# Performance work log

Measured on AMD Instinct MI355X. Metric: run time of the kernel, lower is better.

The kernel has to match this reference:

```python
import jax, jax.numpy as jnp
import numpy as np

KERNEL = 3
STRIDE = 1
PADDING = 1
DILATION = 1
GRID_SIZE = 3
SPLINE_ORDER = 2
IN_CH = 3
OUT_CH = 32
IN_FEAT = IN_CH * KERNEL * KERNEL  # 27
N_BASIS = GRID_SIZE + SPLINE_ORDER  # 5


def _make_grid():
    # efficient-kan grid: uniform knots over [-1, 1] extended by spline_order on each side
    h = 2.0 / GRID_SIZE
    g = np.arange(-SPLINE_ORDER, GRID_SIZE + SPLINE_ORDER + 1, dtype=np.float32) * h - 1.0
    return jnp.asarray(np.broadcast_to(g, (IN_FEAT, g.shape[0])))  # (27, 8)


def b_splines(x, grid):
    # x: (N, F); grid: (F, G). Cox-de Boor recursion.
    x = x[:, :, None]                      # (N, F, 1)
    g = grid[None, :, :]                   # (1, F, G)
    bases = ((x >= g[..., :-1]) & (x < g[..., 1:])).astype(x.dtype)
    for k in range(1, SPLINE_ORDER + 1):
        bases = ((x - g[..., : -(k + 1)]) / (g[..., k:-1] - g[..., : -(k + 1)]) * bases[..., :-1]
                 + (g[..., k + 1:] - x) / (g[..., k + 1:] - g[..., 1:-k]) * bases[..., 1:])
    return bases  # (N, F, N_BASIS)


def setup_inputs() -> dict:
    key = jax.random.key(0)
    k1, k2, k3, k4 = jax.random.split(key, 4)
    x = jax.random.normal(k1, (16, IN_CH, 256, 256), dtype=jnp.float32)
    # Kaiming-ish init scales (values irrelevant for correctness testing)
    base_weight = jax.random.normal(k2, (OUT_CH, IN_FEAT), dtype=jnp.float32) * (1.0 / np.sqrt(IN_FEAT))
    spline_weight = jax.random.normal(k3, (OUT_CH, IN_FEAT, N_BASIS), dtype=jnp.float32) * 0.1
    spline_scaler = jax.random.normal(k4, (OUT_CH, IN_FEAT), dtype=jnp.float32) * (1.0 / np.sqrt(IN_FEAT))
    grid = _make_grid()
    return {"x": x, "base_weight": base_weight, "spline_weight": spline_weight,
            "spline_scaler": spline_scaler, "grid": grid}


def reference(x, base_weight, spline_weight, spline_scaler, grid):
    B, C, H, W = x.shape
    out_h = (H + 2 * PADDING - DILATION * (KERNEL - 1) - 1) // STRIDE + 1
    out_w = (W + 2 * PADDING - DILATION * (KERNEL - 1) - 1) // STRIDE + 1
    # im2col: (B, C*k*k, out_h, out_w), feature ordering (C, kh, kw) matches torch Unfold
    patches = jax.lax.conv_general_dilated_patches(
        x, filter_shape=(KERNEL, KERNEL), window_strides=(STRIDE, STRIDE),
        padding=((PADDING, PADDING), (PADDING, PADDING)), rhs_dilation=(DILATION, DILATION))
    pf = patches.reshape(B, IN_FEAT, out_h * out_w).transpose(0, 2, 1).reshape(-1, IN_FEAT)  # (N, 27)
    # KANLinear: silu base branch + scaled spline branch
    base = jnp.einsum('nf,of->no', jax.nn.silu(pf), base_weight)
    bases = b_splines(pf, grid)                                   # (N, 27, 5)
    scaled_sw = spline_weight * spline_scaler[:, :, None]         # (O, 27, 5)
    spline = jnp.einsum('nfk,ofk->no', bases, scaled_sw)
    out = base + spline                                           # (N, O)
    return out.reshape(B, out_h * out_w, OUT_CH).transpose(0, 2, 1).reshape(B, OUT_CH, out_h, out_w)
```

## Files before the change

### kernel.cpp

```cpp
#include <hip/hip_runtime.h>

#define IN_CH 3
#define OUT_CH 32
#define IN_FEAT 27
#define NB 5
#define NG 8
#define HH 256
#define WW 256
#define NPIX (16 * HH * WW)

#define RECE 24
#define RECP 24
#define TW 66
#define TROWS 6
#define NREC (TROWS * TW)
#define NKS 7
#define WB2_HALVES (NKS * 2 * 64 * 8)
#define WS_NEEDED ((size_t)WB2_HALVES * 2 + 16)
#define SCR_STRIDE 36
#define SCR_WAVE (32 * SCR_STRIDE)

typedef __attribute__((ext_vector_type(8))) _Float16 half8;
typedef __attribute__((ext_vector_type(4))) float f32x4;

__device__ inline void kan_phi6(float xx, const float* g, const float* r1, const float* r2,
                                float* o6) {
    const float sig = 1.0f / (1.0f + __expf(-xx));
    o6[0] = xx * sig;
    float b0[7];
#pragma unroll
    for (int j = 0; j < 7; ++j) b0[j] = (xx >= g[j] && xx < g[j + 1]) ? 1.0f : 0.0f;
    float b1[6];
#pragma unroll
    for (int j = 0; j < 6; ++j)
        b1[j] = (xx - g[j]) * r1[j] * b0[j] + (g[j + 2] - xx) * r1[j + 1] * b0[j + 1];
#pragma unroll
    for (int j = 0; j < NB; ++j)
        o6[1 + j] = (xx - g[j]) * r2[j] * b1[j] + (g[j + 3] - xx) * r2[j + 1] * b1[j + 1];
}

__device__ inline void load_grid(const float* __restrict__ grid, float* g, float* r1, float* r2) {
#pragma unroll
    for (int j = 0; j < NG; ++j) g[j] = grid[j];
#pragma unroll
    for (int j = 0; j < NG - 1; ++j) r1[j] = 1.0f / (g[j + 1] - g[j]);
#pragma unroll
    for (int j = 0; j < NG - 2; ++j) r2[j] = 1.0f / (g[j + 2] - g[j]);
}

__global__ void kan_prepW(const float* __restrict__ bw, const float* __restrict__ sw,
                          const float* __restrict__ ss, const float* __restrict__ grid,
                          _Float16* __restrict__ wb) {
    int t = blockIdx.x * 256 + threadIdx.x;
    if (t >= NKS * 2 * 64) return;

    if (t == 0) {
        float* gt = (float*)(wb + WB2_HALVES);
        gt[0] = grid[0];
        gt[1] = 7.0f / (grid[7] - grid[0]);
    }

    const int lane = t & 63;
    const int nt = (t >> 6) & 1;
    const int kstep = t >> 7;
    const int o = nt * 16 + (lane & 15);
    const int kbase = kstep * 32 + (lane >> 4) * 8;
    half8 v8 = {0, 0, 0, 0, 0, 0, 0, 0};
#pragma unroll
    for (int e = 0; e < 8; ++e) {
        int k = kbase + e;
        float v = 0.0f;
        if (k < 216) {
            int tap = k / 24, within = k % 24;
            if (within < 18) {
                int c = within / 6, j = within % 6;
                int f = c * 9 + tap;
                int of = o * IN_FEAT + f;
                v = (j == 0) ? bw[of] : sw[of * NB + (j - 1)] * ss[of];
            }
        }
        v8[e] = (_Float16)v;
    }
    *(half8*)(wb + (size_t)t * 8) = v8;
}

__global__ __launch_bounds__(256, 4) void kan_fused(const float* __restrict__ x,
                                                    const _Float16* __restrict__ wb,
                                                    float* __restrict__ out) {
    __shared__ _Float16 lPhi[NREC * RECP];
    __shared__ float lScr[4 * SCR_WAVE];

    const int tid = threadIdx.x;
    const int bid = blockIdx.x;
    const int strip = bid & 3;
    const int rowg = (bid >> 2) & 63;
    const int b = bid >> 8;
    const int h0 = rowg * 4;
    const int w0 = strip * 64;

    const int lane = tid & 63;
    const int wid = tid >> 6;
    const int r = lane & 15;
    const int gq = lane >> 4;

    const float* gt = (const float*)(wb + WB2_HALVES);
    const float g0 = gt[0];
    const float invh = gt[1];

    for (int ri = tid; ri < NREC; ri += 256) {
        const int dyR = ri / TW;
        const int wxR = ri - dyR * TW - 1;
        const int hy = h0 + dyR - 1;
        const int wx = w0 + wxR;
        const bool vld = ((unsigned)hy < HH) & ((unsigned)wx < WW);

        _Float16 rec[RECE];
#pragma unroll
        for (int c = 0; c < IN_CH; ++c) {
            const float xx = vld ? x[((b * IN_CH + c) << 16) + (hy << 8) + wx] : 0.0f;
            const float sig = 1.0f / (1.0f + __expf(-xx));
            rec[c * 6] = (_Float16)(xx * sig);
            const float u = (xx - g0) * invh;
            const float fi = floorf(u);
            const int i0 = (int)fi;
            const float t = u - fi;
            const float om = 1.0f - t;
            float wA = 0.5f * om * om;
            float wC = 0.5f * t * t;
            float wB = 1.0f - wA - wC;
            const bool valid = (fi >= 0.0f) & (i0 <= 6);
            wA = valid ? wA : 0.0f;
            wB = valid ? wB : 0.0f;
            wC = valid ? wC : 0.0f;
#pragma unroll
            for (int j = 0; j < NB; ++j) {
                float v = (j == i0 - 2) ? wA : ((j == i0 - 1) ? wB : ((j == i0) ? wC : 0.0f));
                rec[c * 6 + 1 + j] = (_Float16)v;
            }
        }
#pragma unroll
        for (int j = 18; j < RECE; ++j) rec[j] = (_Float16)0.0f;

        half8* dst = (half8*)(lPhi + ri * RECP);
        dst[0] = *(half8*)(rec + 0);
        dst[1] = *(half8*)(rec + 8);
        dst[2] = *(half8*)(rec + 16);
    }
    __syncthreads();

    half8 bf[NKS * 2];
#pragma unroll
    for (int i = 0; i < NKS * 2; ++i)
        bf[i] = *(const half8*)(wb + ((size_t)(i * 64 + lane)) * 8);

    int rowoff[NKS], partoff[NKS];
    bool kvalid[NKS];
#pragma unroll
    for (int k = 0; k < NKS; ++k) {
        const int q = k * 4 + gq;
        const int tap = q / 3;
        const int part = q - tap * 3;
        kvalid[k] = (q < 27);
        const int dyk = tap / 3;
        const int dxk = tap - dyk * 3;
        rowoff[k] = (wid + (kvalid[k] ? dyk : 0)) * TW + (kvalid[k] ? dxk : 0);
        partoff[k] = part * 8;
    }

    const int hrow = h0 + wid;
    float* lT = lScr + wid * SCR_WAVE;
    const int chl = lane >> 3;
    const int pxl = (lane & 7) * 4;

#pragma unroll
    for (int h = 0; h < 2; ++h) {
        f32x4 accA0 = {0.f, 0.f, 0.f, 0.f}, accA1 = {0.f, 0.f, 0.f, 0.f};
        f32x4 accB0 = {0.f, 0.f, 0.f, 0.f}, accB1 = {0.f, 0.f, 0.f, 0.f};
#pragma unroll
        for (int mm = 0; mm < 2; ++mm) {
            const int m = h * 2 + mm;
            half8 a[NKS];
#pragma unroll
            for (int k = 0; k < NKS; ++k) {
                half8 v = {0, 0, 0, 0, 0, 0, 0, 0};
                if (kvalid[k]) {
                    const int ridx = rowoff[k] + m * 16 + r;
                    v = *(const half8*)(lPhi + ridx * RECP + partoff[k]);
                }
                a[k] = v;
            }
            if (mm == 0) {
#pragma unroll
                for (int k = 0; k < NKS; ++k) {
                    accA0 = __builtin_amdgcn_mfma_f32_16x16x32_f16(a[k], bf[k * 2 + 0], accA0, 0, 0, 0);
                    accA1 = __builtin_amdgcn_mfma_f32_16x16x32_f16(a[k], bf[k * 2 + 1], accA1, 0, 0, 0);
                }
            } else {
#pragma unroll
                for (int k = 0; k < NKS; ++k) {
                    accB0 = __builtin_amdgcn_mfma_f32_16x16x32_f16(a[k], bf[k * 2 + 0], accB0, 0, 0, 0);
                    accB1 = __builtin_amdgcn_mfma_f32_16x16x32_f16(a[k], bf[k * 2 + 1], accB1, 0, 0, 0);
                }
            }
        }

        *(f32x4*)(lT + r        * SCR_STRIDE + 0  + gq * 4) = accA0;
        *(f32x4*)(lT + (16 + r) * SCR_STRIDE + 0  + gq * 4) = accA1;
        *(f32x4*)(lT + r        * SCR_STRIDE + 16 + gq * 4) = accB0;
        *(f32x4*)(lT + (16 + r) * SCR_STRIDE + 16 + gq * 4) = accB1;

#pragma unroll
        for (int j = 0; j < 4; ++j) {
            const int ch = j * 8 + chl;
            f32x4 v = *(const f32x4*)(lT + ch * SCR_STRIDE + pxl);
            float* op = out + (((size_t)(b * OUT_CH + ch)) << 16) + (hrow << 8) + w0 + h * 32 + pxl;
            *(f32x4*)op = v;
        }
    }
}

__global__ void kan_combine_weights(const float* __restrict__ bw,
                                    const float* __restrict__ sw,
                                    const float* __restrict__ ss,
                                    float* __restrict__ wc) {
    int idx = blockIdx.x * blockDim.x + threadIdx.x;
    if (idx >= IN_FEAT * 6 * OUT_CH) return;
    int o = idx & 31;
    int j = (idx >> 5) % 6;
    int f = idx / (6 * 32);
    float v;
    if (j == 0) v = bw[o * IN_FEAT + f];
    else        v = sw[(o * IN_FEAT + f) * NB + (j - 1)] * ss[o * IN_FEAT + f];
    wc[idx] = v;
}

__global__ __launch_bounds__(256) void kan_main(const float* __restrict__ x,
                                                const float* __restrict__ grid,
                                                const float* __restrict__ wc,
                                                float* __restrict__ out) {
    const int p = blockIdx.x * blockDim.x + threadIdx.x;
    const int w = p & (WW - 1);
    const int h = (p >> 8) & (HH - 1);
    const int b = p >> 16;
    float g[NG], r1[NG - 1], r2[NG - 2];
    load_grid(grid, g, r1, r2);
    float acc[OUT_CH];
#pragma unroll
    for (int o = 0; o < OUT_CH; ++o) acc[o] = 0.0f;
    const float* xb = x + b * (IN_CH * HH * WW);
    for (int c = 0; c < IN_CH; ++c) {
        const float* xc = xb + c * (HH * WW);
#pragma unroll
        for (int dy = 0; dy < 3; ++dy) {
            const int hy = h + dy - 1;
            const bool vy = (hy >= 0) && (hy < HH);
#pragma unroll
            for (int dx = 0; dx < 3; ++dx) {
                const int wx = w + dx - 1;
                const bool vld = vy && (wx >= 0) && (wx < WW);
                const float xx = vld ? xc[hy * WW + wx] : 0.0f;
                float o6[6];
                kan_phi6(xx, g, r1, r2, o6);
                const float* wf = wc + (c * 9 + dy * 3 + dx) * (6 * OUT_CH);
#pragma unroll
                for (int jj = 0; jj < 6; ++jj) {
                    const float* wj = wf + jj * OUT_CH;
#pragma unroll
                    for (int o = 0; o < OUT_CH; ++o) acc[o] += o6[jj] * wj[o];
                }
            }
        }
    }
    float* ob = out + (size_t)b * (OUT_CH * HH * WW) + h * WW + w;
#pragma unroll
    for (int o = 0; o < OUT_CH; ++o) ob[o * (HH * WW)] = acc[o];
}

extern "C" void kernel_launch(void* const* d_in, const int* in_sizes, int n_in,
                              void* d_out, int out_size, void* d_ws, size_t ws_size,
                              hipStream_t stream) {
    const float* x    = (const float*)d_in[0];
    const float* bw   = (const float*)d_in[1];
    const float* sw   = (const float*)d_in[2];
    const float* ss   = (const float*)d_in[3];
    const float* grid = (const float*)d_in[4];
    float* out = (float*)d_out;

    if (ws_size >= WS_NEEDED) {
        _Float16* wb = (_Float16*)d_ws;
        kan_prepW<<<4, 256, 0, stream>>>(bw, sw, ss, grid, wb);
        kan_fused<<<NPIX / 256, 256, 0, stream>>>(x, wb, out);
    } else {
        float* wc = (float*)d_ws;
        kan_combine_weights<<<(IN_FEAT * 6 * OUT_CH + 255) / 256, 256, 0, stream>>>(bw, sw, ss, wc);
        kan_main<<<NPIX / 256, 256, 0, stream>>>(x, grid, wc, out);
    }
}
```

Baseline: 43.48 us.

## Shrink fused KAN tile to 32-wide strips with 128-thread blocks

Halves the block tile width from 64 to 32 columns and the block size from 256 to 128 threads. Each wave now computes two output rows of 32 pixels instead of one row of 64. The MFMA loop issues each LDS load straight into its MFMA instead of first buffering all seven A fragments, which lowers register pressure. The cost is a larger halo fraction: the 34-wide tile recomputes more border phi values per output, so there is more redundant x loading and spline evaluation in exchange for more, smaller blocks and less LDS per block.

```diff
diff --git a/kernel.cpp b/kernel.cpp
--- a/kernel.cpp
+++ b/kernel.cpp
@@ -11,7 +11,7 @@
 
 #define RECE 24
 #define RECP 24
-#define TW 66
+#define TW 34
 #define TROWS 6
 #define NREC (TROWS * TW)
 #define NKS 7
@@ -84,19 +84,19 @@
     *(half8*)(wb + (size_t)t * 8) = v8;
 }
 
-__global__ __launch_bounds__(256, 4) void kan_fused(const float* __restrict__ x,
+__global__ __launch_bounds__(128, 4) void kan_fused(const float* __restrict__ x,
                                                     const _Float16* __restrict__ wb,
                                                     float* __restrict__ out) {
     __shared__ _Float16 lPhi[NREC * RECP];
-    __shared__ float lScr[4 * SCR_WAVE];
+    __shared__ float lScr[2 * SCR_WAVE];
 
     const int tid = threadIdx.x;
     const int bid = blockIdx.x;
-    const int strip = bid & 3;
-    const int rowg = (bid >> 2) & 63;
-    const int b = bid >> 8;
+    const int strip = bid & 7;
+    const int rowg = (bid >> 3) & 63;
+    const int b = bid >> 9;
     const int h0 = rowg * 4;
-    const int w0 = strip * 64;
+    const int w0 = strip * 32;
 
     const int lane = tid & 63;
     const int wid = tid >> 6;
@@ -107,7 +107,7 @@
     const float g0 = gt[0];
     const float invh = gt[1];
 
-    for (int ri = tid; ri < NREC; ri += 256) {
+    for (int ri = tid; ri < NREC; ri += 128) {
         const int dyR = ri / TW;
         const int wxR = ri - dyR * TW - 1;
         const int hy = h0 + dyR - 1;
@@ -163,43 +163,34 @@
         kvalid[k] = (q < 27);
         const int dyk = tap / 3;
         const int dxk = tap - dyk * 3;
-        rowoff[k] = (wid + (kvalid[k] ? dyk : 0)) * TW + (kvalid[k] ? dxk : 0);
+        rowoff[k] = (kvalid[k] ? dyk : 0) * TW + (kvalid[k] ? dxk : 0);
         partoff[k] = part * 8;
     }
 
-    const int hrow = h0 + wid;
     float* lT = lScr + wid * SCR_WAVE;
     const int chl = lane >> 3;
     const int pxl = (lane & 7) * 4;
 
 #pragma unroll
-    for (int h = 0; h < 2; ++h) {
+    for (int rr = 0; rr < 2; ++rr) {
+        const int row = wid * 2 + rr;
         f32x4 accA0 = {0.f, 0.f, 0.f, 0.f}, accA1 = {0.f, 0.f, 0.f, 0.f};
         f32x4 accB0 = {0.f, 0.f, 0.f, 0.f}, accB1 = {0.f, 0.f, 0.f, 0.f};
 #pragma unroll
-        for (int mm = 0; mm < 2; ++mm) {
-            const int m = h * 2 + mm;
-            half8 a[NKS];
+        for (int m = 0; m < 2; ++m) {
 #pragma unroll
             for (int k = 0; k < NKS; ++k) {
                 half8 v = {0, 0, 0, 0, 0, 0, 0, 0};
                 if (kvalid[k]) {
-                    const int ridx = rowoff[k] + m * 16 + r;
+                    const int ridx = row * TW + rowoff[k] + m * 16 + r;
                     v = *(const half8*)(lPhi + ridx * RECP + partoff[k]);
                 }
-                a[k] = v;
-            }
-            if (mm == 0) {
-#pragma unroll
-                for (int k = 0; k < NKS; ++k) {
-                    accA0 = __builtin_amdgcn_mfma_f32_16x16x32_f16(a[k], bf[k * 2 + 0], accA0, 0, 0, 0);
-                    accA1 = __builtin_amdgcn_mfma_f32_16x16x32_f16(a[k], bf[k * 2 + 1], accA1, 0, 0, 0);
-                }
-            } else {
-#pragma unroll
-                for (int k = 0; k < NKS; ++k) {
-                    accB0 = __builtin_amdgcn_mfma_f32_16x16x32_f16(a[k], bf[k * 2 + 0], accB0, 0, 0, 0);
-                    accB1 = __builtin_amdgcn_mfma_f32_16x16x32_f16(a[k], bf[k * 2 + 1], accB1, 0, 0, 0);
+                if (m == 0) {
+                    accA0 = __builtin_amdgcn_mfma_f32_16x16x32_f16(v, bf[k * 2 + 0], accA0, 0, 0, 0);
+                    accA1 = __builtin_amdgcn_mfma_f32_16x16x32_f16(v, bf[k * 2 + 1], accA1, 0, 0, 0);
+                } else {
+                    accB0 = __builtin_amdgcn_mfma_f32_16x16x32_f16(v, bf[k * 2 + 0], accB0, 0, 0, 0);
+                    accB1 = __builtin_amdgcn_mfma_f32_16x16x32_f16(v, bf[k * 2 + 1], accB1, 0, 0, 0);
                 }
             }
         }
@@ -209,11 +200,12 @@
         *(f32x4*)(lT + r        * SCR_STRIDE + 16 + gq * 4) = accB0;
         *(f32x4*)(lT + (16 + r) * SCR_STRIDE + 16 + gq * 4) = accB1;
 
+        const int hrow = h0 + row;
 #pragma unroll
         for (int j = 0; j < 4; ++j) {
             const int ch = j * 8 + chl;
             f32x4 v = *(const f32x4*)(lT + ch * SCR_STRIDE + pxl);
-            float* op = out + (((size_t)(b * OUT_CH + ch)) << 16) + (hrow << 8) + w0 + h * 32 + pxl;
+            float* op = out + (((size_t)(b * OUT_CH + ch)) << 16) + (hrow << 8) + w0 + pxl;
             *(f32x4*)op = v;
         }
     }
@@ -289,7 +281,7 @@
     if (ws_size >= WS_NEEDED) {
         _Float16* wb = (_Float16*)d_ws;
         kan_prepW<<<4, 256, 0, stream>>>(bw, sw, ss, grid, wb);
-        kan_fused<<<NPIX / 256, 256, 0, stream>>>(x, wb, out);
+        kan_fused<<<NPIX / 128, 128, 0, stream>>>(x, wb, out);
     } else {
         float* wc = (float*)d_ws;
         kan_combine_weights<<<(IN_FEAT * 6 * OUT_CH + 255) / 256, 256, 0, stream>>>(bw, sw, ss, wc);
```

New measurement: 45.39 us. 4.4% more time.
